# Kernel tuning notes

Measured on AMD Instinct MI355X. Metric: run time of the kernel, lower is better.

## Reference

```python
import jax, jax.numpy as jnp
import numpy as np
from jax import lax

SEQ_LENGTH = 32
B, I, O = 1024, 2048, 1024
DT = 1e-3
TAU_PRE, TAU_POST = 0.02, 0.02
ETA_PLUS, ETA_MINUS = 1e-3, 1e-3
W_MIN, W_MAX = -1.0, 1.0
TAU_MEM = 0.02
V_TH = 1.0


def setup_inputs() -> dict:
    key = jax.random.key(0)
    k1, k2, k3 = jax.random.split(key, 3)
    # Bernoulli(0.05) input spikes, rate-coded, reused each timestep
    input_spikes = (jax.random.uniform(k1, (B, I)) < 0.05).astype(jnp.float32)
    weight = jax.random.normal(k2, (O, I), dtype=jnp.float32) * (1.0 / np.sqrt(I))
    bias = jax.random.normal(k3, (O,), dtype=jnp.float32) * 0.01
    return {"input_spikes": input_spikes, "weight": weight, "bias": bias}


def reference(input_spikes, weight, bias):
    decay_pre = jnp.exp(jnp.float32(-DT / TAU_PRE))
    decay_post = jnp.exp(jnp.float32(-DT / TAU_POST))
    v_decay = jnp.exp(jnp.float32(-DT / TAU_MEM))

    b = input_spikes.shape[0]
    v0 = jnp.zeros((b, O), dtype=input_spikes.dtype)
    z0 = jnp.zeros((b, O), dtype=input_spikes.dtype)
    # STDPState(t_pre=1.0, t_post=1.0) broadcast to trace shapes
    tpre0 = jnp.ones((b, I), dtype=input_spikes.dtype)
    tpost0 = jnp.ones((b, O), dtype=input_spikes.dtype)

    def step(carry, _):
        v, w, tpre, tpost, _z = carry
        # linear projection with current (plastic) weights
        z_in = input_spikes @ w.T + bias  # [B, O]
        # LIF output neuron: decay, integrate, threshold, reset
        v = v * v_decay + z_in
        z_out = (v >= V_TH).astype(v.dtype)
        v = v * (1.0 - z_out)
        # STDP trace update: decay then accumulate spikes
        tpre = tpre * decay_pre + input_spikes
        tpost = tpost * decay_post + z_out
        # spike-gated eligibility outer products, summed over batch
        dw = (ETA_PLUS * jnp.einsum('bo,bi->oi', z_out, tpre)
              - ETA_MINUS * jnp.einsum('bo,bi->oi', tpost, input_spikes))
        w = jnp.clip(w + dw, W_MIN, W_MAX)
        return (v, w, tpre, tpost, z_out), None

    (v, w, tpre, tpost, z_out), _ = lax.scan(
        step, (v0, weight, tpre0, tpost0, z0), None, length=SEQ_LENGTH)
    return z_out, v, w
```

## Files before the change

kernel.cpp:

```cpp
#include <hip/hip_runtime.h>
#include <cmath>

#define SEQ 32
#define BB 1024
#define II 2048
#define OO 1024

typedef unsigned short ushortt;

__global__ void build_idx_rev(const float* __restrict__ x, ushortt* __restrict__ idxArr,
                              int* __restrict__ cntArr, int* __restrict__ rcnt,
                              ushortt* __restrict__ rev, ushortt* __restrict__ idxT) {
  int b = blockIdx.x;
  int lane = threadIdx.x;
  __shared__ ushortt sIdx[256];
  const float* row = x + (long)b * II;
  int base = 0;
  for (int c = 0; c < II / 64; ++c) {
    float val = row[c * 64 + lane];
    unsigned long long m = __ballot(val != 0.0f);
    if (val != 0.0f) {
      int pos = base + __popcll(m & ((1ull << lane) - 1ull));
      if (pos < 256) {
        idxArr[(b << 8) + pos] = (ushortt)(c * 64 + lane);
        sIdx[pos] = (ushortt)(c * 64 + lane);
      }
    }
    base += __popcll(m);
  }
  int cnt = base < 256 ? base : 256;
  if (lane == 0) cntArr[b] = cnt;
  __syncthreads();
  {
    int j0 = lane * 4;
    ushort4 u;
    u.x = (j0 + 0 < cnt) ? sIdx[j0 + 0] : (ushortt)II;
    u.y = (j0 + 1 < cnt) ? sIdx[j0 + 1] : (ushortt)II;
    u.z = (j0 + 2 < cnt) ? sIdx[j0 + 2] : (ushortt)II;
    u.w = (j0 + 3 < cnt) ? sIdx[j0 + 3] : (ushortt)II;
    ((ushort4*)idxT)[(lane << 10) + b] = u;
  }
  for (int j = lane; j < cnt; j += 64) {
    int i = sIdx[j];
    int pos = atomicAdd(&rcnt[i], 1);
    if (pos < 128) rev[((long)i << 7) + pos] = (ushortt)b;
  }
}

__global__ void transpose2_f32(const float* __restrict__ zC, const float* __restrict__ vC,
                               float* __restrict__ oz, float* __restrict__ ov) {
  __shared__ float t[32][33];
  const float* src = blockIdx.z ? vC : zC;
  float* dst = blockIdx.z ? ov : oz;
  int c0 = blockIdx.x * 32, r0 = blockIdx.y * 32;
  int tx = threadIdx.x, ty = threadIdx.y;
#pragma unroll
  for (int k = 0; k < 4; k++)
    t[ty + k * 8][tx] = src[(long)(r0 + ty + k * 8) * BB + c0 + tx];
  __syncthreads();
#pragma unroll
  for (int k = 0; k < 4; k++)
    dst[(long)(c0 + ty + k * 8) * OO + r0 + tx] = t[tx][ty + k * 8];
}

__global__ __launch_bounds__(512, 8) void snn_kernel(
    const float* __restrict__ w, const float* __restrict__ bias,
    const ushortt* __restrict__ idxT, const int* __restrict__ cntArr,
    const int* __restrict__ rcnt, const ushortt* __restrict__ rev,
    const ushortt* __restrict__ idxArr,
    float* __restrict__ zC, float* __restrict__ vC, float* __restrict__ outw,
    float dec) {
  int o = blockIdx.x, tid = threadIdx.x, lane = tid & 63, wave = tid >> 6;
  __shared__ float shbuf[8195];
  __shared__ int sCnt, sFlag, cFlag;
  float* wL = shbuf;
  float* aG = shbuf + 2049;
  float* mL = shbuf + 4098;
  int* sList = (int*)(shbuf + 6147);
  float* SnuD = shbuf + 7171;
  float* nT = shbuf + 4098;
  float* Sfix = shbuf + 4098;
  float* SAD = shbuf + 6147;

#pragma unroll
  for (int q = 0; q < 4; ++q) {
    int i = q * 512 + tid;
    wL[i] = w[(long)o * II + i];
    aG[i] = 0.f;
    nT[i] = (float)rcnt[i];
  }
#pragma unroll
  for (int k = 0; k < 2; ++k) SnuD[k * 512 + tid] = 0.f;
  if (tid == 0) {
    sFlag = 0; cFlag = 0;
    wL[II] = 0.f; aG[II] = 0.f; nT[II] = 0.f;
  }

  int jmax[2];
#pragma unroll
  for (int k = 0; k < 2; ++k) {
    int c = cntArr[k * 512 + wave * 64 + lane];
#pragma unroll
    for (int off = 32; off > 0; off >>= 1) c = max(c, __shfl_xor(c, off));
    jmax[k] = c;
  }
  float bo = bias[o];
  unsigned clipped = 0;
  bool everSpk = false;
  float p = 1.f, u = 1.f;
  __syncthreads();

  const ushort4* tpb = (const ushort4*)idxT;
  double S[2];
  float Snu[2], SA[2], v4[2], zk[2];
#pragma unroll
  for (int k = 0; k < 2; ++k) {
    int b = k * 512 + tid;
    double s = 0.0;
    float sn = 0.f;
    int jm4 = (jmax[k] + 3) >> 2;
    const ushort4* tp = tpb + b;
    for (int g = 0; g < jm4; ++g) {
      ushort4 u0 = tp[(g << 10)];
      int a_ = u0.x, b_ = u0.y, c_ = u0.z, d_ = u0.w;
      s += (double)wL[a_]; s += (double)wL[b_]; s += (double)wL[c_]; s += (double)wL[d_];
      sn += nT[a_]; sn += nT[b_]; sn += nT[c_]; sn += nT[d_];
    }
    S[k] = s; Snu[k] = sn;
    SA[k] = 0.f; v4[k] = 0.f; zk[k] = 0.f;
  }
  __syncthreads();
#pragma unroll
  for (int k = 0; k < 2; ++k) {
    int b = k * 512 + tid;
    Sfix[b] = 0.f; SAD[b] = 0.f;
  }

  for (int t = 0; t < SEQ; ++t) {
    p *= dec; u *= dec; u += 1.f;
    float spre = u - p;
    int local = 0;
#pragma unroll
    for (int k = 0; k < 2; ++k) {
      float zin = (float)S[k] + bo;
      float nv = v4[k] * dec + zin;
      float z = (nv >= 1.f) ? 1.f : 0.f;
      nv = nv * (1.f - z);
      v4[k] = nv; zk[k] = z;
      if (z != 0.f) local = 1;
    }
    if (local) sFlag = 1;
    __syncthreads();
    int spk = sFlag;

    if (!spk) {
#pragma unroll
      for (int q = 0; q < 4; ++q) {
        int i = q * 512 + tid;
        bool already = (clipped >> q) & 1u;
        float n = 0.f, atn = 0.f, fix = 0.f;
        bool cl = false;
        if (!already) {
          n = (float)rcnt[i];
          atn = everSpk ? (dec * aG[i]) : 0.f;
          float dw = -(1e-3f * (p * n + atn));
          float wold = wL[i];
          float pre = wold + dw;
          float wv = fminf(fmaxf(pre, -1.f), 1.f);
          cl = (pre <= -1.f);
          if (cl) {
            clipped |= 1u << q;
            fix = (-1.f - wold) - dw;
            if (everSpk) aG[i] = 0.f;
          } else if (everSpk) {
            aG[i] = atn;
          }
          wL[i] = wv;
        }
        unsigned long long m = __ballot(cl);
        if (m) {
          if (lane == 0) cFlag = 1;
          while (m) {
            int src = __builtin_ctzll(m);
            m &= m - 1;
            int ii = __shfl(i, src);
            float fx = __shfl(fix, src);
            float mn = -__shfl(n, src);
            float ma = -__shfl(atn, src);
            int rc = rcnt[ii];
            const ushortt* rp = rev + ((long)ii << 7);
            for (int r = lane; r < rc; r += 64) {
              int b2 = rp[r];
              atomicAdd(&Sfix[b2], fx);
              atomicAdd(&SnuD[b2], mn);
              if (everSpk) atomicAdd(&SAD[b2], ma);
            }
          }
        }
      }
      __syncthreads();
      float coefP = 1e-3f * p;
      if (cFlag) {
#pragma unroll
        for (int k = 0; k < 2; ++k) {
          int b = k * 512 + tid;
          S[k] = S[k] - (double)coefP * (double)Snu[k]
                      - (double)1e-3f * (double)(dec * SA[k])
                      + (double)Sfix[b];
          SA[k] = dec * SA[k] + SAD[b];
          Snu[k] = Snu[k] + SnuD[b];
          Sfix[b] = 0.f; SnuD[b] = 0.f; SAD[b] = 0.f;
        }
      } else {
#pragma unroll
        for (int k = 0; k < 2; ++k) {
          S[k] = S[k] - (double)coefP * (double)Snu[k]
                      - (double)1e-3f * (double)(dec * SA[k]);
          SA[k] = dec * SA[k];
        }
      }
      if (tid == 0) { sFlag = 0; cFlag = 0; }
      __syncthreads();
    } else {
      everSpk = true;
      if (tid == 0) sCnt = 0;
      __syncthreads();
#pragma unroll
      for (int k = 0; k < 2; ++k)
        if (zk[k] != 0.f) { int pos = atomicAdd(&sCnt, 1); sList[pos] = k * 512 + tid; }
#pragma unroll
      for (int q = 0; q < 4; ++q) mL[q * 512 + tid] = 0.f;
      __syncthreads();
      int ns = sCnt;
      for (int s = wave; s < ns; s += 8) {
        int b = sList[s];
        int cb = cntArr[b];
        const ushortt* ip = idxArr + (b << 8);
        for (int j = lane; j < cb; j += 64)
          atomicAdd(&mL[ip[j]], 1.f);
      }
      __syncthreads();
      float cv = (float)ns;
#pragma unroll
      for (int q = 0; q < 4; ++q) {
        int i = q * 512 + tid;
        float mt = mL[i];
        float atn = dec * aG[i] + mt;
        float n = (float)rcnt[i];
        float dw = 1e-3f * (p * cv + spre * mt) - 1e-3f * (p * n + atn);
        float wold = wL[i];
        float pre = wold + dw;
        float wv = fminf(fmaxf(pre, -1.f), 1.f);
        bool cl = (pre <= -1.f);
        bool was = (clipped >> q) & 1u;
        if (cl) clipped |= 1u << q; else clipped &= ~(1u << q);
        wL[i] = wv;
        aG[i] = cl ? 0.f : atn;
        bool flip = (cl != was);
        float dn = cl ? -n : n;
        unsigned long long m = __ballot(flip);
        while (m) {
          int src = __builtin_ctzll(m);
          m &= m - 1;
          int ii = __shfl(i, src);
          float d = __shfl(dn, src);
          int rc = rcnt[ii];
          const ushortt* rp = rev + ((long)ii << 7);
          for (int r = lane; r < rc; r += 64)
            atomicAdd(&SnuD[rp[r]], d);
        }
      }
      __syncthreads();
#pragma unroll
      for (int k = 0; k < 2; ++k) {
        int b = k * 512 + tid;
        double s = 0.0;
        float sa = 0.f;
        int jm4 = (jmax[k] + 3) >> 2;
        const ushort4* tp = tpb + b;
        for (int g = 0; g < jm4; ++g) {
          ushort4 u0 = tp[(g << 10)];
          int a_ = u0.x, b_ = u0.y, c_ = u0.z, d_ = u0.w;
          s += (double)wL[a_]; sa += aG[a_];
          s += (double)wL[b_]; sa += aG[b_];
          s += (double)wL[c_]; sa += aG[c_];
          s += (double)wL[d_]; sa += aG[d_];
        }
        S[k] = s; SA[k] = sa;
        Snu[k] = Snu[k] + SnuD[b];
        SnuD[b] = 0.f;
        Sfix[b] = 0.f; SAD[b] = 0.f;
      }
      if (tid == 0) { sFlag = 0; cFlag = 0; }
      __syncthreads();
    }
  }

  __syncthreads();
#pragma unroll
  for (int q = 0; q < 4; ++q) outw[(long)o * II + q * 512 + tid] = wL[q * 512 + tid];
#pragma unroll
  for (int k = 0; k < 2; ++k) {
    int b = k * 512 + tid;
    zC[(long)o * BB + b] = zk[k];
    vC[(long)o * BB + b] = v4[k];
  }
}

extern "C" void kernel_launch(void* const* d_in, const int* in_sizes, int n_in,
                              void* d_out, int out_size, void* d_ws, size_t ws_size,
                              hipStream_t stream) {
  const float* x = (const float*)d_in[0];
  const float* w = (const float*)d_in[1];
  const float* bias = (const float*)d_in[2];
  float* out = (float*)d_out;

  char* ws = (char*)d_ws;
  ushortt* idxArr = (ushortt*)(ws + 0);
  int* cntArr = (int*)(ws + 524288);
  ushortt* idxT = (ushortt*)(ws + 528384);
  int* rcnt = (int*)(ws + 1060864);
  ushortt* rev = (ushortt*)(ws + 1069056);
  float* zC = (float*)(ws + 1593344);
  float* vC = (float*)(ws + 5787648);

  hipMemsetAsync(rcnt, 0, II * sizeof(int), stream);
  build_idx_rev<<<BB, 64, 0, stream>>>(x, idxArr, cntArr, rcnt, rev, idxT);

  const float dec = (float)exp(-0.05);

  snn_kernel<<<OO, 512, 0, stream>>>(w, bias, idxT, cntArr, rcnt, rev, idxArr,
                                     zC, vC, out + 2 * BB * OO, dec);

  transpose2_f32<<<dim3(BB / 32, OO / 32, 2), dim3(32, 8), 0, stream>>>(zC, vC, out, out + BB * OO);
}
```

Measured before the change: 276.9 us.

## Interleave weight and trace in float2 LDS, per-thread loop bounds, split accumulators

Packs the per-input weight and eligibility trace into one float2 shared array, so each gather fetches both with a single LDS load. The gather loops now use each thread's own spike count instead of the wave maximum, and they split the sums across two accumulators to shorten the double-precision add dependency chain. rcnt values are cached in registers instead of being re-read from global memory each step. This changes summation order in the double accumulation. The restructured LDS aliasing could raise bank conflicts on the strided float2 accesses.

```diff
diff --git a/kernel.cpp b/kernel.cpp
--- a/kernel.cpp
+++ b/kernel.cpp
@@ -71,39 +71,36 @@
     float* __restrict__ zC, float* __restrict__ vC, float* __restrict__ outw,
     float dec) {
   int o = blockIdx.x, tid = threadIdx.x, lane = tid & 63, wave = tid >> 6;
-  __shared__ float shbuf[8195];
+  __shared__ float2 wa[II + 1];
+  __shared__ float mLb[II + 1];
+  __shared__ int sList[BB];
+  __shared__ float SnuD[BB];
   __shared__ int sCnt, sFlag, cFlag;
-  float* wL = shbuf;
-  float* aG = shbuf + 2049;
-  float* mL = shbuf + 4098;
-  int* sList = (int*)(shbuf + 6147);
-  float* SnuD = shbuf + 7171;
-  float* nT = shbuf + 4098;
-  float* Sfix = shbuf + 4098;
-  float* SAD = shbuf + 6147;
-
+  float* mL = mLb;
+  float* nT = mLb;
+  float* Sfix = mLb;
+  float* SAD = (float*)sList;
+
+  float n4[4];
 #pragma unroll
   for (int q = 0; q < 4; ++q) {
     int i = q * 512 + tid;
-    wL[i] = w[(long)o * II + i];
-    aG[i] = 0.f;
-    nT[i] = (float)rcnt[i];
+    float nv = (float)rcnt[i];
+    wa[i] = make_float2(w[(long)o * II + i], 0.f);
+    nT[i] = nv;
+    n4[q] = nv;
   }
 #pragma unroll
   for (int k = 0; k < 2; ++k) SnuD[k * 512 + tid] = 0.f;
+  int cb[2];
+#pragma unroll
+  for (int k = 0; k < 2; ++k) cb[k] = cntArr[k * 512 + tid];
   if (tid == 0) {
     sFlag = 0; cFlag = 0;
-    wL[II] = 0.f; aG[II] = 0.f; nT[II] = 0.f;
-  }
-
-  int jmax[2];
-#pragma unroll
-  for (int k = 0; k < 2; ++k) {
-    int c = cntArr[k * 512 + wave * 64 + lane];
-#pragma unroll
-    for (int off = 32; off > 0; off >>= 1) c = max(c, __shfl_xor(c, off));
-    jmax[k] = c;
-  }
+    wa[II] = make_float2(0.f, 0.f);
+    nT[II] = 0.f;
+  }
+
   float bo = bias[o];
   unsigned clipped = 0;
   bool everSpk = false;
@@ -116,17 +113,18 @@
 #pragma unroll
   for (int k = 0; k < 2; ++k) {
     int b = k * 512 + tid;
-    double s = 0.0;
-    float sn = 0.f;
-    int jm4 = (jmax[k] + 3) >> 2;
+    double s0 = 0.0, s1 = 0.0;
+    float sn0 = 0.f, sn1 = 0.f;
+    int jm4 = (cb[k] + 3) >> 2;
     const ushort4* tp = tpb + b;
     for (int g = 0; g < jm4; ++g) {
       ushort4 u0 = tp[(g << 10)];
-      int a_ = u0.x, b_ = u0.y, c_ = u0.z, d_ = u0.w;
-      s += (double)wL[a_]; s += (double)wL[b_]; s += (double)wL[c_]; s += (double)wL[d_];
-      sn += nT[a_]; sn += nT[b_]; sn += nT[c_]; sn += nT[d_];
+      s0 += (double)wa[u0.x].x; sn0 += nT[u0.x];
+      s1 += (double)wa[u0.y].x; sn1 += nT[u0.y];
+      s0 += (double)wa[u0.z].x; sn0 += nT[u0.z];
+      s1 += (double)wa[u0.w].x; sn1 += nT[u0.w];
     }
-    S[k] = s; Snu[k] = sn;
+    S[k] = s0 + s1; Snu[k] = sn0 + sn1;
     SA[k] = 0.f; v4[k] = 0.f; zk[k] = 0.f;
   }
   __syncthreads();
@@ -161,21 +159,20 @@
         float n = 0.f, atn = 0.f, fix = 0.f;
         bool cl = false;
         if (!already) {
-          n = (float)rcnt[i];
-          atn = everSpk ? (dec * aG[i]) : 0.f;
+          float2 tq = wa[i];
+          n = n4[q];
+          atn = everSpk ? (dec * tq.y) : 0.f;
           float dw = -(1e-3f * (p * n + atn));
-          float wold = wL[i];
-          float pre = wold + dw;
+          float pre = tq.x + dw;
           float wv = fminf(fmaxf(pre, -1.f), 1.f);
           cl = (pre <= -1.f);
           if (cl) {
             clipped |= 1u << q;
-            fix = (-1.f - wold) - dw;
-            if (everSpk) aG[i] = 0.f;
-          } else if (everSpk) {
-            aG[i] = atn;
+            fix = (-1.f - tq.x) - dw;
+            wa[i] = make_float2(wv, 0.f);
+          } else {
+            wa[i] = make_float2(wv, atn);
           }
-          wL[i] = wv;
         }
         unsigned long long m = __ballot(cl);
         if (m) {
@@ -234,9 +231,9 @@
       int ns = sCnt;
       for (int s = wave; s < ns; s += 8) {
         int b = sList[s];
-        int cb = cntArr[b];
+        int cbb = cntArr[b];
         const ushortt* ip = idxArr + (b << 8);
-        for (int j = lane; j < cb; j += 64)
+        for (int j = lane; j < cbb; j += 64)
           atomicAdd(&mL[ip[j]], 1.f);
       }
       __syncthreads();
@@ -244,18 +241,17 @@
 #pragma unroll
       for (int q = 0; q < 4; ++q) {
         int i = q * 512 + tid;
+        float2 tq = wa[i];
         float mt = mL[i];
-        float atn = dec * aG[i] + mt;
-        float n = (float)rcnt[i];
+        float atn = dec * tq.y + mt;
+        float n = n4[q];
         float dw = 1e-3f * (p * cv + spre * mt) - 1e-3f * (p * n + atn);
-        float wold = wL[i];
-        float pre = wold + dw;
+        float pre = tq.x + dw;
         float wv = fminf(fmaxf(pre, -1.f), 1.f);
         bool cl = (pre <= -1.f);
         bool was = (clipped >> q) & 1u;
         if (cl) clipped |= 1u << q; else clipped &= ~(1u << q);
-        wL[i] = wv;
-        aG[i] = cl ? 0.f : atn;
+        wa[i] = make_float2(wv, cl ? 0.f : atn);
         bool flip = (cl != was);
         float dn = cl ? -n : n;
         unsigned long long m = __ballot(flip);
@@ -274,19 +270,19 @@
 #pragma unroll
       for (int k = 0; k < 2; ++k) {
         int b = k * 512 + tid;
-        double s = 0.0;
-        float sa = 0.f;
-        int jm4 = (jmax[k] + 3) >> 2;
+        double s0 = 0.0, s1 = 0.0;
+        float sa0 = 0.f, sa1 = 0.f;
+        int jm4 = (cb[k] + 3) >> 2;
         const ushort4* tp = tpb + b;
         for (int g = 0; g < jm4; ++g) {
           ushort4 u0 = tp[(g << 10)];
-          int a_ = u0.x, b_ = u0.y, c_ = u0.z, d_ = u0.w;
-          s += (double)wL[a_]; sa += aG[a_];
-          s += (double)wL[b_]; sa += aG[b_];
-          s += (double)wL[c_]; sa += aG[c_];
-          s += (double)wL[d_]; sa += aG[d_];
-        }
-        S[k] = s; SA[k] = sa;
+          float2 e0 = wa[u0.x], e1 = wa[u0.y], e2 = wa[u0.z], e3 = wa[u0.w];
+          s0 += (double)e0.x; sa0 += e0.y;
+          s1 += (double)e1.x; sa1 += e1.y;
+          s0 += (double)e2.x; sa0 += e2.y;
+          s1 += (double)e3.x; sa1 += e3.y;
+        }
+        S[k] = s0 + s1; SA[k] = sa0 + sa1;
         Snu[k] = Snu[k] + SnuD[b];
         SnuD[b] = 0.f;
         Sfix[b] = 0.f; SAD[b] = 0.f;
@@ -298,7 +294,7 @@
 
   __syncthreads();
 #pragma unroll
-  for (int q = 0; q < 4; ++q) outw[(long)o * II + q * 512 + tid] = wL[q * 512 + tid];
+  for (int q = 0; q < 4; ++q) outw[(long)o * II + q * 512 + tid] = wa[q * 512 + tid].x;
 #pragma unroll
   for (int k = 0; k < 2; ++k) {
     int b = k * 512 + tid;
```

Measured after the change: 283.8 us. 2.5% more time.
